# Performance work log

Hardware: AMD Instinct MI355X
Metric: run time of the kernel (lower is better)

Reference implementation:

```python
import jax, jax.numpy as jnp
import numpy as np

D_MODEL = 1024
N_HEADS = 16
HEAD_DIM = D_MODEL // N_HEADS  # 64


def setup_inputs() -> dict:
    key = jax.random.key(0)
    ks = jax.random.split(key, 6)
    scale_in = 1.0 / np.sqrt(D_MODEL)
    scale_hd = 1.0 / np.sqrt(N_HEADS * HEAD_DIM)
    inputs_q = jax.random.normal(ks[0], (4, 2048, D_MODEL), dtype=jnp.float32)
    # DenseGeneral kernels: [d_model, n_heads, head_dim] for q/k/v, [n_heads, head_dim, d_model] for out.
    Wq = jax.random.normal(ks[1], (D_MODEL, N_HEADS, HEAD_DIM), dtype=jnp.float32) * scale_in
    Wk = jax.random.normal(ks[2], (D_MODEL, N_HEADS, HEAD_DIM), dtype=jnp.float32) * scale_in
    Wv = jax.random.normal(ks[3], (D_MODEL, N_HEADS, HEAD_DIM), dtype=jnp.float32) * scale_in
    Wo = jax.random.normal(ks[4], (N_HEADS, HEAD_DIM, D_MODEL), dtype=jnp.float32) * scale_hd
    bq = jnp.zeros((N_HEADS, HEAD_DIM), dtype=jnp.float32)
    bk = jnp.zeros((N_HEADS, HEAD_DIM), dtype=jnp.float32)
    bv = jnp.zeros((N_HEADS, HEAD_DIM), dtype=jnp.float32)
    bo = jnp.zeros((D_MODEL,), dtype=jnp.float32)
    return {"inputs_q": inputs_q, "Wq": Wq, "bq": bq, "Wk": Wk, "bk": bk,
            "Wv": Wv, "bv": bv, "Wo": Wo, "bo": bo}


def reference(inputs_q, Wq, bq, Wk, bk, Wv, bv, Wo, bo):
    # Self-attention: inputs_kv = inputs_q.
    # QKV projections (DenseGeneral axis=-1 -> (heads, head_dim)).
    q = jnp.einsum('bsf,fhd->bshd', inputs_q, Wq) + bq  # [B,S,H,D]
    k = jnp.einsum('bsf,fhd->bshd', inputs_q, Wk) + bk
    v = jnp.einsum('bsf,fhd->bshd', inputs_q, Wv) + bv
    # Scaled dot-product attention (naive: full [B,H,S,S] scores, as in source).
    q = q / jnp.sqrt(jnp.asarray(HEAD_DIM, dtype=q.dtype))
    scores = jnp.einsum('bqhd,bkhd->bhqk', q, k)  # [B,H,Sq,Sk]
    attn = jax.nn.softmax(scores, axis=-1)
    x = jnp.einsum('bhqk,bkhd->bqhd', attn, v)  # [B,S,H,D]
    # Output projection over (heads, head_dim).
    out = jnp.einsum('bqhd,hdf->bqf', x, Wo) + bo  # [B,S,d_model]
    return out
```

## Files before the change

### kernel.cpp

```cpp
#include <hip/hip_runtime.h>
#include <math.h>

typedef __bf16 bf16;
typedef __attribute__((ext_vector_type(4))) __bf16 bf16x4;
typedef __attribute__((ext_vector_type(8))) __bf16 bf16x8;
typedef __attribute__((ext_vector_type(4))) float f32x4;

#define LOG2E 1.44269504088896340736f

__device__ __forceinline__ f32x4 mfma16(bf16x8 a, bf16x8 b, f32x4 c) {
  return __builtin_amdgcn_mfma_f32_16x16x32_bf16(a, b, c, 0, 0, 0);
}

__device__ __forceinline__ void load_lds16(const bf16* g, bf16* l) {
  __builtin_amdgcn_global_load_lds(
      (__attribute__((address_space(1))) void*)(g),
      (__attribute__((address_space(3))) void*)(l), 16, 0, 0);
}

__global__ __launch_bounds__(256) void prep(
    const float* __restrict__ x, const float* __restrict__ Wq,
    const float* __restrict__ Wk, const float* __restrict__ Wv,
    const float* __restrict__ Wo, bf16* __restrict__ xb,
    bf16* __restrict__ Wcat, bf16* __restrict__ WoT, float qscale) {
  __shared__ float t[32][33];
  const int z = blockIdx.z;
  const int tid = threadIdx.x;
  if (z == 4) {
    const int blk = blockIdx.y * 32 + blockIdx.x;
    const int base = blk * 8192;
#pragma unroll
    for (int u = 0; u < 4; u++) {
      int i = base + u * 2048 + tid * 8;
      float4 a = *(const float4*)&x[i];
      float4 b = *(const float4*)&x[i + 4];
      bf16x8 v;
      v[0] = (bf16)a.x; v[1] = (bf16)a.y; v[2] = (bf16)a.z; v[3] = (bf16)a.w;
      v[4] = (bf16)b.x; v[5] = (bf16)b.y; v[6] = (bf16)b.z; v[7] = (bf16)b.w;
      *(bf16x8*)&xb[i] = v;
    }
  } else {
    const float* src = (z == 0) ? Wq : (z == 1) ? Wk : (z == 2) ? Wv : Wo;
    bf16* dst = (z == 3) ? WoT : (Wcat + (size_t)z * 1024 * 1024);
    const float scale = (z == 0) ? qscale : 1.0f;
    const int tx = tid & 31, ty = tid >> 5;
    int c0 = blockIdx.x * 32, r0 = blockIdx.y * 32;
    for (int i = ty; i < 32; i += 8)
      t[i][tx] = src[(r0 + i) * 1024 + c0 + tx];
    __syncthreads();
    for (int i = ty; i < 32; i += 8)
      dst[(c0 + i) * 1024 + r0 + tx] = (bf16)(t[tx][i] * scale);
  }
}

__global__ __launch_bounds__(512, 2) void gemm_qkv(
    const bf16* __restrict__ A, const bf16* __restrict__ Bt,
    bf16* __restrict__ Qo, bf16* __restrict__ Ko, bf16* __restrict__ Vo,
    const float* __restrict__ b0, const float* __restrict__ b1,
    const float* __restrict__ b2) {
  __shared__ bf16 lA[2][256 * 64];
  __shared__ bf16 lB[2][192 * 64];
  const int tid = threadIdx.x;
  const int lane = tid & 63, w = tid >> 6;
  const int l16 = lane & 15, quad = lane >> 4;
  const int rswz = l16 & 7;
  const int wm = w >> 2, wn = w & 3;
  const int id = blockIdx.x;
  const int xcd = id & 7, local = id >> 3;
  const int m0 = (xcd * 4 + (local & 3)) * 256;
  const int n0 = (local >> 2) * 192;

  const bf16* aSrc[4];
  const bf16* bSrc[3];
  int aDst[4], bDst[3];
#pragma unroll
  for (int li = 0; li < 4; li++) {
    int s = li * 512 + tid;
    int r = s >> 3, c = (s & 7) ^ (r & 7);
    aSrc[li] = A + (size_t)(m0 + r) * 1024 + c * 8;
    aDst[li] = (li * 512 + w * 64) * 8;
  }
#pragma unroll
  for (int li = 0; li < 3; li++) {
    int s = li * 512 + tid;
    int r = s >> 3, c = (s & 7) ^ (r & 7);
    bSrc[li] = Bt + (size_t)(n0 + r) * 1024 + c * 8;
    bDst[li] = (li * 512 + w * 64) * 8;
  }

#pragma unroll
  for (int li = 0; li < 4; li++) load_lds16(aSrc[li], &lA[0][aDst[li]]);
#pragma unroll
  for (int li = 0; li < 3; li++) load_lds16(bSrc[li], &lB[0][bDst[li]]);

  f32x4 acc[8][3] = {};
  for (int t = 0; t < 16; t++) {
    const int p = t & 1;
    if (t < 15) {
      const int k1 = (t + 1) * 64;
#pragma unroll
      for (int li = 0; li < 4; li++)
        load_lds16(aSrc[li] + k1, &lA[p ^ 1][aDst[li]]);
      asm volatile("s_waitcnt vmcnt(4)" ::: "memory");
    } else {
      asm volatile("s_waitcnt vmcnt(0)" ::: "memory");
    }
    __builtin_amdgcn_s_barrier();
    __builtin_amdgcn_sched_barrier(0);

    {
      bf16x8 af[8], bfr[3];
#pragma unroll
      for (int i = 0; i < 8; i++)
        af[i] = *(const bf16x8*)&lA[p][(wm * 128 + i * 16 + l16) * 64 + (quad ^ rswz) * 8];
#pragma unroll
      for (int j = 0; j < 3; j++)
        bfr[j] = *(const bf16x8*)&lB[p][(wn * 48 + j * 16 + l16) * 64 + (quad ^ rswz) * 8];
#pragma unroll
      for (int i = 0; i < 8; i++)
#pragma unroll
        for (int j = 0; j < 3; j++)
          acc[i][j] = mfma16(bfr[j], af[i], acc[i][j]);
    }

    if (t < 15) {
      const int k1 = (t + 1) * 64;
#pragma unroll
      for (int li = 0; li < 3; li++)
        load_lds16(bSrc[li] + k1, &lB[p ^ 1][bDst[li]]);
    }

    {
      bf16x8 af[8], bfr[3];
#pragma unroll
      for (int i = 0; i < 8; i++)
        af[i] = *(const bf16x8*)&lA[p][(wm * 128 + i * 16 + l16) * 64 + ((4 + quad) ^ rswz) * 8];
#pragma unroll
      for (int j = 0; j < 3; j++)
        bfr[j] = *(const bf16x8*)&lB[p][(wn * 48 + j * 16 + l16) * 64 + ((4 + quad) ^ rswz) * 8];
#pragma unroll
      for (int i = 0; i < 8; i++)
#pragma unroll
        for (int j = 0; j < 3; j++)
          acc[i][j] = mfma16(bfr[j], af[i], acc[i][j]);
    }

    asm volatile("" ::: "memory");
    __builtin_amdgcn_s_barrier();
  }

#pragma unroll
  for (int j = 0; j < 3; j++) {
    const int nn = n0 + wn * 48 + j * 16 + quad * 4;
    const int which = nn >> 10;
    bf16* dst = (which == 0) ? Qo : (which == 1) ? Ko : Vo;
    const float* bsrc = (which == 0) ? b0 : (which == 1) ? b1 : b2;
    const float bscale = (which == 0) ? (0.125f * LOG2E) : 1.0f;
    const int nl = nn & 1023;
    const int h = nl >> 6, d0 = nl & 63;
    float4 bv4 = *(const float4*)&bsrc[nl];
#pragma unroll
    for (int i = 0; i < 8; i++) {
      const int grow = m0 + wm * 128 + i * 16 + l16;
      const int bb = grow >> 11, sq = grow & 2047;
      const size_t hb = (size_t)(bb * 16 + h) * 131072;
      if (which != 2) {
        bf16x4 pw;
        pw[0] = (bf16)(acc[i][j][0] + bv4.x * bscale);
        pw[1] = (bf16)(acc[i][j][1] + bv4.y * bscale);
        pw[2] = (bf16)(acc[i][j][2] + bv4.z * bscale);
        pw[3] = (bf16)(acc[i][j][3] + bv4.w * bscale);
        *(bf16x4*)&dst[hb + (size_t)sq * 64 + d0] = pw;
      } else {
        dst[hb + (size_t)(d0 + 0) * 2048 + sq] = (bf16)(acc[i][j][0] + bv4.x);
        dst[hb + (size_t)(d0 + 1) * 2048 + sq] = (bf16)(acc[i][j][1] + bv4.y);
        dst[hb + (size_t)(d0 + 2) * 2048 + sq] = (bf16)(acc[i][j][2] + bv4.z);
        dst[hb + (size_t)(d0 + 3) * 2048 + sq] = (bf16)(acc[i][j][3] + bv4.w);
      }
    }
  }
}

template <int MODE>
__global__ __launch_bounds__(256, 3) void gemm_bt(
    const bf16* __restrict__ A, const bf16* __restrict__ Bt, int N, int K,
    bf16* __restrict__ Qo, bf16* __restrict__ Ko, bf16* __restrict__ Vo,
    const float* __restrict__ b0, const float* __restrict__ b1,
    const float* __restrict__ b2,
    float* __restrict__ Co, const float* __restrict__ bias) {
  __shared__ bf16 lA[2][128 * 32];
  __shared__ bf16 lB[2][128 * 32];
  const int tid = threadIdx.x;
  const int lane = tid & 63, w = tid >> 6;
  const int l16 = lane & 15, quad = lane >> 4;
  const int swz = (l16 >> 2) & 3;
  const int wm = w >> 1, wn = w & 1;
  const int id = blockIdx.x;
  const int xcd = id & 7, local = id >> 3;
  const int m0 = (xcd * 8 + (local & 7)) * 128;
  const int n0 = (local >> 3) * 128;

  const int srow = w * 16 + (lane >> 2);
  const int scol = (((lane & 3) ^ ((lane >> 4) & 3)) * 8);
  const bf16* Ag = A + (size_t)(m0 + srow) * K + scol;
  const bf16* Bg = Bt + (size_t)(n0 + srow) * K + scol;
  const int ldw = w * 16 * 32;

  load_lds16(Ag, &lA[0][ldw]);
  load_lds16(Ag + (size_t)64 * K, &lA[0][ldw + 64 * 32]);
  load_lds16(Bg, &lB[0][ldw]);
  load_lds16(Bg + (size_t)64 * K, &lB[0][ldw + 64 * 32]);

  f32x4 acc[4][4] = {};
  for (int k0 = 0; k0 < K; k0 += 32) {
    const int p = (k0 >> 5) & 1;
    __syncthreads();
    if (k0 + 32 < K) {
      load_lds16(Ag + k0 + 32, &lA[p ^ 1][ldw]);
      load_lds16(Ag + k0 + 32 + (size_t)64 * K, &lA[p ^ 1][ldw + 64 * 32]);
      load_lds16(Bg + k0 + 32, &lB[p ^ 1][ldw]);
      load_lds16(Bg + k0 + 32 + (size_t)64 * K, &lB[p ^ 1][ldw + 64 * 32]);
    }
    bf16x8 af[4], bfr[4];
#pragma unroll
    for (int i = 0; i < 4; i++)
      af[i] = *(const bf16x8*)&lA[p][(wm * 64 + i * 16 + l16) * 32 + (quad ^ swz) * 8];
#pragma unroll
    for (int i = 0; i < 4; i++)
      bfr[i] = *(const bf16x8*)&lB[p][(wn * 64 + i * 16 + l16) * 32 + (quad ^ swz) * 8];
#pragma unroll
    for (int i = 0; i < 4; i++)
#pragma unroll
      for (int j = 0; j < 4; j++)
        acc[i][j] = mfma16(bfr[j], af[i], acc[i][j]);
  }

  {
#pragma unroll
    for (int j = 0; j < 4; j++) {
      const int gcol = n0 + wn * 64 + j * 16 + quad * 4;
      float4 bv4 = *(const float4*)&bias[gcol];
#pragma unroll
      for (int i = 0; i < 4; i++) {
        const int grow = m0 + wm * 64 + i * 16 + l16;
        f32x4 v = acc[i][j];
        v[0] += bv4.x; v[1] += bv4.y; v[2] += bv4.z; v[3] += bv4.w;
        *(f32x4*)&Co[(size_t)grow * N + gcol] = v;
      }
    }
  }
}

__global__ __launch_bounds__(256, 2) void attn(const bf16* __restrict__ Q,
                                               const bf16* __restrict__ Kb,
                                               const bf16* __restrict__ Vt,
                                               bf16* __restrict__ X2) {
  __shared__ bf16 lK[2][2][64][32];
  __shared__ bf16 lV[2][2][64][32];
  __shared__ bf16 lP[4][64][72];
  const int tid = threadIdx.x;
  const int lane = tid & 63, w = tid >> 6;
  const int l16 = lane & 15, quad = lane >> 4;
  const int swz = (l16 >> 2) & 3;
  const int bh = blockIdx.x & 63;
  const int q0 = (blockIdx.x >> 6) * 256;
  const int bb = bh >> 4, h = bh & 15;
  const size_t base = (size_t)bh * 2048 * 64;

  bf16x8 aq[4][2];
#pragma unroll
  for (int mi = 0; mi < 4; mi++)
#pragma unroll
    for (int kh = 0; kh < 2; kh++)
      aq[mi][kh] = *(const bf16x8*)&Q[base + (size_t)(q0 + w * 64 + mi * 16 + l16) * 64 + kh * 32 + quad * 8];

  f32x4 o_acc[4][4] = {};
  float l_r[4] = {0.f, 0.f, 0.f, 0.f};

  const int drow = lane >> 2;
  const int dcol = (((lane & 3) ^ ((lane >> 4) & 3)) * 8);
  const bf16* Kg = Kb + base + (size_t)(w * 16 + drow) * 64 + dcol;
  const bf16* Vg = Vt + base + (size_t)(w * 16 + drow) * 2048 + dcol;

  load_lds16(Kg, &lK[0][0][w * 16][0]);
  load_lds16(Kg + 32, &lK[0][1][w * 16][0]);
  load_lds16(Vg, &lV[0][0][w * 16][0]);
  load_lds16(Vg + 32, &lV[0][1][w * 16][0]);

  for (int kt = 0; kt < 32; kt++) {
    const int p = kt & 1;
    __syncthreads();
    if (kt + 1 < 32) {
      const bf16* kg = Kg + (size_t)(kt + 1) * 64 * 64;
      const bf16* vg = Vg + (kt + 1) * 64;
      load_lds16(kg, &lK[p ^ 1][0][w * 16][0]);
      load_lds16(kg + 32, &lK[p ^ 1][1][w * 16][0]);
      load_lds16(vg, &lV[p ^ 1][0][w * 16][0]);
      load_lds16(vg + 32, &lV[p ^ 1][1][w * 16][0]);
    }

#pragma unroll
    for (int g = 0; g < 2; g++) {
      f32x4 s[2][4] = {};
#pragma unroll
      for (int n2 = 0; n2 < 2; n2++) {
        const int ni = g * 2 + n2;
        bf16x8 ak0 = *(const bf16x8*)&lK[p][0][ni * 16 + l16][(quad ^ swz) * 8];
        bf16x8 ak1 = *(const bf16x8*)&lK[p][1][ni * 16 + l16][(quad ^ swz) * 8];
#pragma unroll
        for (int mi = 0; mi < 4; mi++) {
          s[n2][mi] = mfma16(ak0, aq[mi][0], s[n2][mi]);
          s[n2][mi] = mfma16(ak1, aq[mi][1], s[n2][mi]);
        }
      }
#pragma unroll
      for (int n2 = 0; n2 < 2; n2++) {
        const int ni = g * 2 + n2;
#pragma unroll
        for (int mi = 0; mi < 4; mi++) {
          bf16x4 pw;
          float lp = 0.f;
#pragma unroll
          for (int rg = 0; rg < 4; rg++) {
            float pv = __builtin_amdgcn_exp2f(s[n2][mi][rg]);
            lp += pv;
            pw[rg] = (bf16)pv;
          }
          l_r[mi] += lp;
          *(bf16x4*)&lP[w][mi * 16 + l16][ni * 16 + quad * 4] = pw;
        }
      }
    }

    bf16x8 vf0[4], vf1[4];
#pragma unroll
    for (int di = 0; di < 4; di++) {
      vf0[di] = *(const bf16x8*)&lV[p][0][di * 16 + l16][(quad ^ swz) * 8];
      vf1[di] = *(const bf16x8*)&lV[p][1][di * 16 + l16][(quad ^ swz) * 8];
    }
#pragma unroll
    for (int mi = 0; mi < 4; mi++) {
      bf16x8 ap0 = *(const bf16x8*)&lP[w][mi * 16 + l16][quad * 8];
      bf16x8 ap1 = *(const bf16x8*)&lP[w][mi * 16 + l16][32 + quad * 8];
#pragma unroll
      for (int di = 0; di < 4; di++) {
        o_acc[mi][di] = mfma16(ap0, vf0[di], o_acc[mi][di]);
        o_acc[mi][di] = mfma16(ap1, vf1[di], o_acc[mi][di]);
      }
    }
  }

#pragma unroll
  for (int mi = 0; mi < 4; mi++) {
    float l = l_r[mi];
    l += __shfl_xor(l, 16);
    l += __shfl_xor(l, 32);
    l_r[mi] = 1.f / l;
  }
#pragma unroll
  for (int mi = 0; mi < 4; mi++)
#pragma unroll
    for (int rg = 0; rg < 4; rg++) {
      float inv = __shfl(l_r[mi], quad * 4 + rg);
      int s = q0 + w * 64 + mi * 16 + quad * 4 + rg;
#pragma unroll
      for (int di = 0; di < 4; di++) {
        float v = o_acc[mi][di][rg] * inv;
        X2[((size_t)bb * 2048 + s) * 1024 + h * 64 + di * 16 + l16] = (bf16)v;
      }
    }
}

extern "C" void kernel_launch(void* const* d_in, const int* in_sizes, int n_in,
                              void* d_out, int out_size, void* d_ws, size_t ws_size,
                              hipStream_t stream) {
  const float* x  = (const float*)d_in[0];
  const float* Wq = (const float*)d_in[1];
  const float* bq = (const float*)d_in[2];
  const float* Wk = (const float*)d_in[3];
  const float* bk = (const float*)d_in[4];
  const float* Wv = (const float*)d_in[5];
  const float* bv = (const float*)d_in[6];
  const float* Wo = (const float*)d_in[7];
  const float* bo = (const float*)d_in[8];
  float* out = (float*)d_out;

  char* ws = (char*)d_ws;
  bf16* Xb   = (bf16*)(ws);
  bf16* Wcat = (bf16*)(ws + 16777216);
  bf16* WoT  = (bf16*)(ws + 23068672);
  bf16* Qb   = (bf16*)(ws + 25165824);
  bf16* Kbf  = (bf16*)(ws + 41943040);
  bf16* Vt   = (bf16*)(ws + 58720256);
  bf16* X2   = Xb;

  prep<<<dim3(32, 32, 5), 256, 0, stream>>>(
      x, Wq, Wk, Wv, Wo, Xb, Wcat, WoT, 0.125f * LOG2E);

  gemm_qkv<<<512, 512, 0, stream>>>(Xb, Wcat, Qb, Kbf, Vt, bq, bk, bv);

  attn<<<512, 256, 0, stream>>>(Qb, Kbf, Vt, X2);

  gemm_bt<1><<<512, 256, 0, stream>>>(X2, WoT, 1024, 1024,
      nullptr, nullptr, nullptr, nullptr, nullptr, nullptr, out, bo);
}
```

Baseline: 275.7 us.

## Restructure QKV GEMM main loop into four-phase interleaved LDS/MFMA schedule with setprio

The QKV projection GEMM inner loop is split into four quadrant phases (rows 0-3 by cols 0-1, rows 0-3 by col 2, rows 4-7 by col 2, rows 4-7 by cols 0-1). Each phase interleaves LDS fragment reads and a slice of the next tile's global-to-LDS loads with barriers, and raises wave priority around MFMA clusters, in the style of ping-pong scheduling. The goal is to overlap LDS reads and global prefetch with matrix math and to lower register pressure, since only half of the A fragments are live at once. In exchange it adds two extra barriers per iteration and a full vmcnt(0) wait at the top of each iteration. Both LDS buffers are still overwritten while other waves may still be reading the current buffer, so correctness relies on the barrier placement.

```diff
diff --git a/kernel.cpp b/kernel.cpp
--- a/kernel.cpp
+++ b/kernel.cpp
@@ -96,57 +96,96 @@
   f32x4 acc[8][3] = {};
   for (int t = 0; t < 16; t++) {
     const int p = t & 1;
+    const int k1 = (t + 1) * 64;
+    bf16x8 af[2][4], bfr[2][2], bfr2[2];
+
+    asm volatile("s_waitcnt vmcnt(0)" ::: "memory");
+    __builtin_amdgcn_s_barrier();
+#pragma unroll
+    for (int ks = 0; ks < 2; ks++) {
+#pragma unroll
+      for (int i = 0; i < 4; i++)
+        af[ks][i] = *(const bf16x8*)&lA[p][(wm * 128 + i * 16 + l16) * 64 + ((ks * 4 + quad) ^ rswz) * 8];
+#pragma unroll
+      for (int j = 0; j < 2; j++)
+        bfr[ks][j] = *(const bf16x8*)&lB[p][(wn * 48 + j * 16 + l16) * 64 + ((ks * 4 + quad) ^ rswz) * 8];
+    }
+    asm volatile("s_waitcnt lgkmcnt(0)" ::: "memory");
+    __builtin_amdgcn_sched_barrier(0);
+    __builtin_amdgcn_s_setprio(1);
+#pragma unroll
+    for (int ks = 0; ks < 2; ks++)
+#pragma unroll
+      for (int i = 0; i < 4; i++)
+#pragma unroll
+        for (int j = 0; j < 2; j++)
+          acc[i][j] = mfma16(bfr[ks][j], af[ks][i], acc[i][j]);
+    __builtin_amdgcn_s_setprio(0);
+    __builtin_amdgcn_sched_barrier(0);
+
+#pragma unroll
+    for (int ks = 0; ks < 2; ks++)
+      bfr2[ks] = *(const bf16x8*)&lB[p][(wn * 48 + 32 + l16) * 64 + ((ks * 4 + quad) ^ rswz) * 8];
     if (t < 15) {
-      const int k1 = (t + 1) * 64;
-#pragma unroll
-      for (int li = 0; li < 4; li++)
-        load_lds16(aSrc[li] + k1, &lA[p ^ 1][aDst[li]]);
-      asm volatile("s_waitcnt vmcnt(4)" ::: "memory");
-    } else {
-      asm volatile("s_waitcnt vmcnt(0)" ::: "memory");
+      load_lds16(aSrc[0] + k1, &lA[p ^ 1][aDst[0]]);
+      load_lds16(aSrc[1] + k1, &lA[p ^ 1][aDst[1]]);
     }
     __builtin_amdgcn_s_barrier();
-    __builtin_amdgcn_sched_barrier(0);
-
-    {
-      bf16x8 af[8], bfr[3];
-#pragma unroll
-      for (int i = 0; i < 8; i++)
-        af[i] = *(const bf16x8*)&lA[p][(wm * 128 + i * 16 + l16) * 64 + (quad ^ rswz) * 8];
-#pragma unroll
-      for (int j = 0; j < 3; j++)
-        bfr[j] = *(const bf16x8*)&lB[p][(wn * 48 + j * 16 + l16) * 64 + (quad ^ rswz) * 8];
-#pragma unroll
-      for (int i = 0; i < 8; i++)
-#pragma unroll
-        for (int j = 0; j < 3; j++)
-          acc[i][j] = mfma16(bfr[j], af[i], acc[i][j]);
-    }
-
+    asm volatile("s_waitcnt lgkmcnt(0)" ::: "memory");
+    __builtin_amdgcn_sched_barrier(0);
+    __builtin_amdgcn_s_setprio(1);
+#pragma unroll
+    for (int ks = 0; ks < 2; ks++)
+#pragma unroll
+      for (int i = 0; i < 4; i++)
+        acc[i][2] = mfma16(bfr2[ks], af[ks][i], acc[i][2]);
+    __builtin_amdgcn_s_setprio(0);
+    __builtin_amdgcn_sched_barrier(0);
+
+#pragma unroll
+    for (int ks = 0; ks < 2; ks++)
+#pragma unroll
+      for (int i = 0; i < 4; i++)
+        af[ks][i] = *(const bf16x8*)&lA[p][(wm * 128 + (4 + i) * 16 + l16) * 64 + ((ks * 4 + quad) ^ rswz) * 8];
     if (t < 15) {
-      const int k1 = (t + 1) * 64;
-#pragma unroll
-      for (int li = 0; li < 3; li++)
-        load_lds16(bSrc[li] + k1, &lB[p ^ 1][bDst[li]]);
-    }
-
-    {
-      bf16x8 af[8], bfr[3];
-#pragma unroll
-      for (int i = 0; i < 8; i++)
-        af[i] = *(const bf16x8*)&lA[p][(wm * 128 + i * 16 + l16) * 64 + ((4 + quad) ^ rswz) * 8];
-#pragma unroll
-      for (int j = 0; j < 3; j++)
-        bfr[j] = *(const bf16x8*)&lB[p][(wn * 48 + j * 16 + l16) * 64 + ((4 + quad) ^ rswz) * 8];
-#pragma unroll
-      for (int i = 0; i < 8; i++)
-#pragma unroll
-        for (int j = 0; j < 3; j++)
-          acc[i][j] = mfma16(bfr[j], af[i], acc[i][j]);
-    }
-
-    asm volatile("" ::: "memory");
+      load_lds16(aSrc[2] + k1, &lA[p ^ 1][aDst[2]]);
+      load_lds16(aSrc[3] + k1, &lA[p ^ 1][aDst[3]]);
+    }
     __builtin_amdgcn_s_barrier();
+    asm volatile("s_waitcnt lgkmcnt(0)" ::: "memory");
+    __builtin_amdgcn_sched_barrier(0);
+    __builtin_amdgcn_s_setprio(1);
+#pragma unroll
+    for (int ks = 0; ks < 2; ks++)
+#pragma unroll
+      for (int i = 0; i < 4; i++)
+        acc[4 + i][2] = mfma16(bfr2[ks], af[ks][i], acc[4 + i][2]);
+    __builtin_amdgcn_s_setprio(0);
+    __builtin_amdgcn_sched_barrier(0);
+
+#pragma unroll
+    for (int ks = 0; ks < 2; ks++)
+#pragma unroll
+      for (int j = 0; j < 2; j++)
+        bfr[ks][j] = *(const bf16x8*)&lB[p][(wn * 48 + j * 16 + l16) * 64 + ((ks * 4 + quad) ^ rswz) * 8];
+    if (t < 15) {
+      load_lds16(bSrc[0] + k1, &lB[p ^ 1][bDst[0]]);
+      load_lds16(bSrc[1] + k1, &lB[p ^ 1][bDst[1]]);
+      load_lds16(bSrc[2] + k1, &lB[p ^ 1][bDst[2]]);
+    }
+    __builtin_amdgcn_s_barrier();
+    asm volatile("s_waitcnt lgkmcnt(0)" ::: "memory");
+    __builtin_amdgcn_sched_barrier(0);
+    __builtin_amdgcn_s_setprio(1);
+#pragma unroll
+    for (int ks = 0; ks < 2; ks++)
+#pragma unroll
+      for (int i = 0; i < 4; i++)
+#pragma unroll
+        for (int j = 0; j < 2; j++)
+          acc[4 + i][j] = mfma16(bfr[ks][j], af[ks][i], acc[4 + i][j]);
+    __builtin_amdgcn_s_setprio(0);
+    __builtin_amdgcn_sched_barrier(0);
   }
 
 #pragma unroll
```

After: 277.0 us. Within noise of the previous version (+0.5%).
